# Optimization experiments

Measured on AMD Instinct MI355X. Metric: run time of the kernel, lower is better.

Reference implementation:

```python
import jax, jax.numpy as jnp
import numpy as np


def _normal_distance(n1, n2):
    # Cosine-style normal distance: 1 - <n1, n2>. The original module stubs
    # this as 0; we use the canonical mesh-normal loss so the cdist+argmin+
    # gather chain is exercised end-to-end.
    return 1.0 - jnp.sum(n1 * n2, axis=-1)


def setup_inputs() -> dict:
    key = jax.random.key(0)
    k1, k2, k3, k4 = jax.random.split(key, 4)
    N, M = 8192, 32768
    pred_pts = jax.random.normal(k1, (1, N, 3), dtype=jnp.float32)
    pred_nrm = jax.random.normal(k2, (1, N, 3), dtype=jnp.float32)
    gt_pts = jax.random.normal(k3, (1, M, 3), dtype=jnp.float32)
    gt_nrm = jax.random.normal(k4, (1, M, 3), dtype=jnp.float32)
    # unit normals, as on a real mesh
    pred_nrm = pred_nrm / jnp.linalg.norm(pred_nrm, axis=-1, keepdims=True)
    gt_nrm = gt_nrm / jnp.linalg.norm(gt_nrm, axis=-1, keepdims=True)
    return {
        "predicted_points_batch": pred_pts,
        "predicted_normals_batch": pred_nrm,
        "gt_points_batch": gt_pts,
        "gt_normals_batch": gt_nrm,
    }


def reference(predicted_points_batch, predicted_normals_batch,
              gt_points_batch, gt_normals_batch):
    # Original forward returns inside the first loop iteration -> element 0 only.
    p = predicted_points_batch[0]    # [N,3]
    pn = predicted_normals_batch[0]  # [N,3]
    g = gt_points_batch[0]           # [M,3]
    gn = gt_normals_batch[0]         # [M,3]

    # Squared pairwise distances (monotone in true cdist; only argmin is used).
    # d2[i,j] = |p_i|^2 + |g_j|^2 - 2 p_i . g_j   -> one [N,M] intermediate.
    d2 = (jnp.sum(p * p, axis=1)[:, None]
          + jnp.sum(g * g, axis=1)[None, :]
          - 2.0 * (p @ g.T))                      # [N,M]

    gt_idx = jnp.argmin(d2, axis=1)    # nearest gt point per predicted point, [N]
    pr_idx = jnp.argmin(d2, axis=0)    # nearest predicted point per gt point, [M]

    nearest_gt_normals = gn[gt_idx]    # [N,3]
    nearest_pr_normals = pn[pr_idx]    # [M,3]

    dist1 = _normal_distance(pn, nearest_gt_normals)  # [N]
    dist2 = _normal_distance(gn, nearest_pr_normals)  # [M]
    return jnp.mean(dist1) + jnp.mean(dist2)
```

## Files before the change

### kernel.cpp

```cpp
#include <hip/hip_runtime.h>
#include <stdint.h>
#include <float.h>

#define BLK 256
#define IPT 8
#define OWNERS (BLK * IPT)
#define SLICE 128
#define SUB 64
#define FBLK 64

typedef unsigned long long ull;
typedef float v2f __attribute__((ext_vector_type(2)));

__device__ __forceinline__ v2f fma2(v2f a, v2f b, v2f c) {
    return __builtin_elementwise_fma(a, b, c);
}

__device__ __forceinline__ unsigned int ford(float f) {
    int b = __float_as_int(f);
    return (b >= 0) ? ((unsigned)b ^ 0x80000000u) : ~(unsigned)b;
}
__device__ __forceinline__ float ford_inv(unsigned int u) {
    int b = (u & 0x80000000u) ? (int)(u ^ 0x80000000u) : (int)~u;
    return __int_as_float(b);
}

__global__ __launch_bounds__(BLK) void nn_min_dual(
    const float* __restrict__ p, const float* __restrict__ g,
    ull* __restrict__ rowmin, ull* __restrict__ colmin,
    float* __restrict__ out, int rowBlocks, int rowSlices, int colSlices)
{
    __shared__ float sbx[SLICE], sby[SLICE], sbz[SLICE], sbw[SLICE];

    if (blockIdx.x == 0 && threadIdx.x == 0) *out = 0.0f;

    const float* A; const float* B; ull* outmin; int id, nSlices;
    if ((int)blockIdx.x < rowBlocks) {
        id = blockIdx.x;             A = p; B = g; outmin = rowmin; nSlices = rowSlices;
    } else {
        id = blockIdx.x - rowBlocks; A = g; B = p; outmin = colmin; nSlices = colSlices;
    }
    const int chunk = id / nSlices;
    const int slice = id - chunk * nSlices;
    const int s0 = slice * SLICE;

    if (threadIdx.x < SLICE) {
        int s = s0 + threadIdx.x;
        float bx = B[3 * s], by = B[3 * s + 1], bz = B[3 * s + 2];
        float w = fmaf(bz, bz, fmaf(by, by, bx * bx));
        sbx[threadIdx.x] = bx; sby[threadIdx.x] = by;
        sbz[threadIdx.x] = bz; sbw[threadIdx.x] = w;
    }

    const int o0 = chunk * OWNERS + threadIdx.x;
    v2f ax2[IPT], ay2[IPT], az2[IPT];
    float best[IPT];
    int base[IPT];
#pragma unroll
    for (int r = 0; r < IPT; ++r) {
        int o = o0 + r * BLK;
        float axv = -2.0f * A[3 * o];
        float ayv = -2.0f * A[3 * o + 1];
        float azv = -2.0f * A[3 * o + 2];
        ax2[r] = (v2f){axv, axv};
        ay2[r] = (v2f){ayv, ayv};
        az2[r] = (v2f){azv, azv};
        best[r] = FLT_MAX;
        base[r] = s0;
    }
    __syncthreads();

    for (int st = 0; st < SLICE; st += SUB) {
        float prev[IPT];
#pragma unroll
        for (int r = 0; r < IPT; ++r) prev[r] = best[r];
#pragma unroll 2
        for (int k = st; k < st + SUB; k += 2) {
            v2f qx = *(const v2f*)&sbx[k];
            v2f qy = *(const v2f*)&sby[k];
            v2f qz = *(const v2f*)&sbz[k];
            v2f qw = *(const v2f*)&sbw[k];
#pragma unroll
            for (int r = 0; r < IPT; ++r) {
                v2f t = fma2(az2[r], qz, qw);
                t = fma2(ay2[r], qy, t);
                t = fma2(ax2[r], qx, t);
                best[r] = fminf(fminf(t.x, t.y), best[r]);
            }
        }
#pragma unroll
        for (int r = 0; r < IPT; ++r)
            if (best[r] < prev[r]) base[r] = s0 + st;
    }

#pragma unroll
    for (int r = 0; r < IPT; ++r) {
        ull packed = ((ull)ford(best[r]) << 32) | (unsigned)base[r];
        atomicMin(&outmin[o0 + r * BLK], packed);
    }
}

__global__ __launch_bounds__(FBLK) void finalize_kernel(
    const ull* __restrict__ rowmin, const ull* __restrict__ colmin,
    const float* __restrict__ p, const float* __restrict__ g,
    const float* __restrict__ pn, const float* __restrict__ gn,
    float* __restrict__ out, int N, int M, float invN, float invM)
{
    int t = blockIdx.x * FBLK + threadIdx.x;
    float c = 0.0f;
    if (t < N + M) {
        const float* A; const float* B; const float* An; const float* Bn;
        ull packed; int o; float inv;
        if (t < N) { o = t;     A = p; B = g; An = pn; Bn = gn; packed = rowmin[o]; inv = invN; }
        else       { o = t - N; A = g; B = p; An = gn; Bn = pn; packed = colmin[o]; inv = invM; }

        float ax = -2.0f * A[3 * o];
        float ay = -2.0f * A[3 * o + 1];
        float az = -2.0f * A[3 * o + 2];
        float bestf = ford_inv((unsigned int)(packed >> 32));
        int b0 = (int)(packed & 0xffffffffull);

        int idx = 0x7fffffff;
#pragma unroll 4
        for (int jj = 0; jj < SUB; ++jj) {
            int s = b0 + jj;
            float bx = B[3 * s], by = B[3 * s + 1], bz = B[3 * s + 2];
            float w = fmaf(bz, bz, fmaf(by, by, bx * bx));
            float v = fmaf(ax, bx, fmaf(ay, by, fmaf(az, bz, w)));
            int cand = (v == bestf) ? s : 0x7fffffff;
            idx = (cand < idx) ? cand : idx;
        }
        if (idx == 0x7fffffff) idx = b0;

        float d = An[3 * o] * Bn[3 * idx] + An[3 * o + 1] * Bn[3 * idx + 1]
                + An[3 * o + 2] * Bn[3 * idx + 2];
        c = (1.0f - d) * inv;
    }
#pragma unroll
    for (int off = 32; off > 0; off >>= 1) c += __shfl_down(c, off, 64);
    if (threadIdx.x == 0) atomicAdd(out, c);
}

extern "C" void kernel_launch(void* const* d_in, const int* in_sizes, int n_in,
                              void* d_out, int out_size, void* d_ws, size_t ws_size,
                              hipStream_t stream) {
    const float* p  = (const float*)d_in[0];
    const float* pn = (const float*)d_in[1];
    const float* g  = (const float*)d_in[2];
    const float* gn = (const float*)d_in[3];
    const int N = in_sizes[0] / 3;
    const int M = in_sizes[2] / 3;
    float* out = (float*)d_out;

    ull* rowmin = (ull*)d_ws;
    ull* colmin = rowmin + N;

    hipMemsetAsync(d_ws, 0xFF, (size_t)(N + M) * sizeof(ull), stream);

    const int rowSlices = M / SLICE;
    const int colSlices = N / SLICE;
    const int rowBlocks = (N / OWNERS) * rowSlices;
    const int colBlocks = (M / OWNERS) * colSlices;
    nn_min_dual<<<rowBlocks + colBlocks, BLK, 0, stream>>>(
        p, g, rowmin, colmin, out, rowBlocks, rowSlices, colSlices);

    const int tot = N + M;
    finalize_kernel<<<(tot + FBLK - 1) / FBLK, FBLK, 0, stream>>>(
        rowmin, colmin, p, g, pn, gn, out, N, M, 1.0f / N, 1.0f / M);
}
```

Baseline: 116.0 us.

## Replace atomicMin reduction with per-group partial minima and a reduce pass

The scan kernel now has each block loop over multiple staged slices of the other point set and write its per-owner packed minimum to a dedicated workspace slot instead of issuing global atomicMin. A separate reduce kernel takes the minimum across the K partial groups before the existing exact-index recovery and normal-distance sum. This removes the memset and millions of 64-bit atomics and reduces redundant per-block loading of owner coordinates. In exchange it needs a large workspace and extra reduce-pass reads, and it keeps the old path as a fallback when geometry or workspace size does not fit.

```diff
diff --git a/kernel.cpp b/kernel.cpp
--- a/kernel.cpp
+++ b/kernel.cpp
@@ -5,8 +5,10 @@
 #define BLK 256
 #define IPT 8
 #define OWNERS (BLK * IPT)
-#define SLICE 128
+#define SLICE 256
 #define SUB 64
+#define KROW 64
+#define KCOL 32
 #define FBLK 64
 
 typedef unsigned long long ull;
@@ -25,32 +27,28 @@
     return __int_as_float(b);
 }
 
-__global__ __launch_bounds__(BLK) void nn_min_dual(
-    const float* __restrict__ p, const float* __restrict__ g,
-    ull* __restrict__ rowmin, ull* __restrict__ colmin,
-    float* __restrict__ out, int rowBlocks, int rowSlices, int colSlices)
+__global__ __launch_bounds__(BLK) void nn_scan(
+    const float* __restrict__ p, const float* __restrict__ g,
+    ull* __restrict__ wsR, ull* __restrict__ wsC,
+    float* __restrict__ out, int N, int M)
 {
     __shared__ float sbx[SLICE], sby[SLICE], sbz[SLICE], sbw[SLICE];
 
     if (blockIdx.x == 0 && threadIdx.x == 0) *out = 0.0f;
 
-    const float* A; const float* B; ull* outmin; int id, nSlices;
+    const int rowChunks = N / OWNERS;
+    const int rowBlocks = rowChunks * KROW;
+
+    const float* A; const float* B; ull* ws; int id, nK, NO, cpb;
     if ((int)blockIdx.x < rowBlocks) {
-        id = blockIdx.x;             A = p; B = g; outmin = rowmin; nSlices = rowSlices;
+        id = blockIdx.x;             A = p; B = g; ws = wsR; nK = KROW; NO = N; cpb = M / KROW;
     } else {
-        id = blockIdx.x - rowBlocks; A = g; B = p; outmin = colmin; nSlices = colSlices;
-    }
-    const int chunk = id / nSlices;
-    const int slice = id - chunk * nSlices;
-    const int s0 = slice * SLICE;
-
-    if (threadIdx.x < SLICE) {
-        int s = s0 + threadIdx.x;
-        float bx = B[3 * s], by = B[3 * s + 1], bz = B[3 * s + 2];
-        float w = fmaf(bz, bz, fmaf(by, by, bx * bx));
-        sbx[threadIdx.x] = bx; sby[threadIdx.x] = by;
-        sbz[threadIdx.x] = bz; sbw[threadIdx.x] = w;
-    }
+        id = blockIdx.x - rowBlocks; A = g; B = p; ws = wsC; nK = KCOL; NO = M; cpb = N / KCOL;
+    }
+    const int chunk = id / nK;
+    const int kgrp  = id - chunk * nK;
+    const int c0 = kgrp * cpb;
+    const int nStages = cpb / SLICE;
 
     const int o0 = chunk * OWNERS + threadIdx.x;
     v2f ax2[IPT], ay2[IPT], az2[IPT];
@@ -66,42 +64,54 @@
         ay2[r] = (v2f){ayv, ayv};
         az2[r] = (v2f){azv, azv};
         best[r] = FLT_MAX;
-        base[r] = s0;
-    }
-    __syncthreads();
-
-    for (int st = 0; st < SLICE; st += SUB) {
-        float prev[IPT];
-#pragma unroll
-        for (int r = 0; r < IPT; ++r) prev[r] = best[r];
+        base[r] = c0;
+    }
+
+    for (int stage = 0; stage < nStages; ++stage) {
+        const int gs0 = c0 + stage * SLICE;
+        if (stage) __syncthreads();
+
+        {
+            int s = gs0 + threadIdx.x;
+            float bx = B[3 * s], by = B[3 * s + 1], bz = B[3 * s + 2];
+            float w = fmaf(bz, bz, fmaf(by, by, bx * bx));
+            sbx[threadIdx.x] = bx; sby[threadIdx.x] = by;
+            sbz[threadIdx.x] = bz; sbw[threadIdx.x] = w;
+        }
+        __syncthreads();
+
+        for (int st = 0; st < SLICE; st += SUB) {
+            float prev[IPT];
+#pragma unroll
+            for (int r = 0; r < IPT; ++r) prev[r] = best[r];
 #pragma unroll 2
-        for (int k = st; k < st + SUB; k += 2) {
-            v2f qx = *(const v2f*)&sbx[k];
-            v2f qy = *(const v2f*)&sby[k];
-            v2f qz = *(const v2f*)&sbz[k];
-            v2f qw = *(const v2f*)&sbw[k];
-#pragma unroll
-            for (int r = 0; r < IPT; ++r) {
-                v2f t = fma2(az2[r], qz, qw);
-                t = fma2(ay2[r], qy, t);
-                t = fma2(ax2[r], qx, t);
-                best[r] = fminf(fminf(t.x, t.y), best[r]);
+            for (int k = st; k < st + SUB; k += 2) {
+                v2f qx = *(const v2f*)&sbx[k];
+                v2f qy = *(const v2f*)&sby[k];
+                v2f qz = *(const v2f*)&sbz[k];
+                v2f qw = *(const v2f*)&sbw[k];
+#pragma unroll
+                for (int r = 0; r < IPT; ++r) {
+                    v2f t = fma2(az2[r], qz, qw);
+                    t = fma2(ay2[r], qy, t);
+                    t = fma2(ax2[r], qx, t);
+                    best[r] = fminf(fminf(t.x, t.y), best[r]);
+                }
             }
-        }
-#pragma unroll
-        for (int r = 0; r < IPT; ++r)
-            if (best[r] < prev[r]) base[r] = s0 + st;
-    }
-
-#pragma unroll
-    for (int r = 0; r < IPT; ++r) {
-        ull packed = ((ull)ford(best[r]) << 32) | (unsigned)base[r];
-        atomicMin(&outmin[o0 + r * BLK], packed);
-    }
-}
-
-__global__ __launch_bounds__(FBLK) void finalize_kernel(
-    const ull* __restrict__ rowmin, const ull* __restrict__ colmin,
+#pragma unroll
+            for (int r = 0; r < IPT; ++r)
+                if (best[r] < prev[r]) base[r] = gs0 + st;
+        }
+    }
+
+    ull* dst = ws + (size_t)kgrp * NO;
+#pragma unroll
+    for (int r = 0; r < IPT; ++r)
+        dst[o0 + r * BLK] = ((ull)ford(best[r]) << 32) | (unsigned)base[r];
+}
+
+__global__ __launch_bounds__(FBLK) void nn_reduce(
+    const ull* __restrict__ wsR, const ull* __restrict__ wsC,
     const float* __restrict__ p, const float* __restrict__ g,
     const float* __restrict__ pn, const float* __restrict__ gn,
     float* __restrict__ out, int N, int M, float invN, float invM)
@@ -110,15 +120,22 @@
     float c = 0.0f;
     if (t < N + M) {
         const float* A; const float* B; const float* An; const float* Bn;
-        ull packed; int o; float inv;
-        if (t < N) { o = t;     A = p; B = g; An = pn; Bn = gn; packed = rowmin[o]; inv = invN; }
-        else       { o = t - N; A = g; B = p; An = gn; Bn = pn; packed = colmin[o]; inv = invM; }
+        const ull* ws; int o, K, NO; float inv;
+        if (t < N) { o = t;     A = p; B = g; An = pn; Bn = gn; ws = wsR; K = KROW; NO = N; inv = invN; }
+        else       { o = t - N; A = g; B = p; An = gn; Bn = pn; ws = wsC; K = KCOL; NO = M; inv = invM; }
+
+        ull bestp = ws[o];
+#pragma unroll 4
+        for (int k = 1; k < K; ++k) {
+            ull v2 = ws[(size_t)k * NO + o];
+            bestp = (v2 < bestp) ? v2 : bestp;
+        }
 
         float ax = -2.0f * A[3 * o];
         float ay = -2.0f * A[3 * o + 1];
         float az = -2.0f * A[3 * o + 2];
-        float bestf = ford_inv((unsigned int)(packed >> 32));
-        int b0 = (int)(packed & 0xffffffffull);
+        float bestf = ford_inv((unsigned int)(bestp >> 32));
+        int b0 = (int)(bestp & 0xffffffffull);
 
         int idx = 0x7fffffff;
 #pragma unroll 4
@@ -132,6 +149,105 @@
         }
         if (idx == 0x7fffffff) idx = b0;
 
+        float d = An[3 * o] * Bn[3 * idx] + An[3 * o + 1] * Bn[3 * idx + 1]
+                + An[3 * o + 2] * Bn[3 * idx + 2];
+        c = (1.0f - d) * inv;
+    }
+#pragma unroll
+    for (int off = 32; off > 0; off >>= 1) c += __shfl_down(c, off, 64);
+    if (threadIdx.x == 0) atomicAdd(out, c);
+}
+
+#define L_SLICE 128
+
+__global__ __launch_bounds__(BLK) void nn_min_dual(
+    const float* __restrict__ p, const float* __restrict__ g,
+    ull* __restrict__ rowmin, ull* __restrict__ colmin,
+    float* __restrict__ out, int rowBlocks, int rowSlices, int colSlices)
+{
+    __shared__ float sbx[L_SLICE], sby[L_SLICE], sbz[L_SLICE], sbw[L_SLICE];
+    if (blockIdx.x == 0 && threadIdx.x == 0) *out = 0.0f;
+    const float* A; const float* B; ull* outmin; int id, nSlices;
+    if ((int)blockIdx.x < rowBlocks) {
+        id = blockIdx.x;             A = p; B = g; outmin = rowmin; nSlices = rowSlices;
+    } else {
+        id = blockIdx.x - rowBlocks; A = g; B = p; outmin = colmin; nSlices = colSlices;
+    }
+    const int chunk = id / nSlices;
+    const int slice = id - chunk * nSlices;
+    const int s0 = slice * L_SLICE;
+    if (threadIdx.x < L_SLICE) {
+        int s = s0 + threadIdx.x;
+        float bx = B[3 * s], by = B[3 * s + 1], bz = B[3 * s + 2];
+        float w = fmaf(bz, bz, fmaf(by, by, bx * bx));
+        sbx[threadIdx.x] = bx; sby[threadIdx.x] = by;
+        sbz[threadIdx.x] = bz; sbw[threadIdx.x] = w;
+    }
+    const int o0 = chunk * OWNERS + threadIdx.x;
+    v2f ax2[IPT], ay2[IPT], az2[IPT];
+    float best[IPT]; int base[IPT];
+#pragma unroll
+    for (int r = 0; r < IPT; ++r) {
+        int o = o0 + r * BLK;
+        float axv = -2.0f * A[3 * o], ayv = -2.0f * A[3 * o + 1], azv = -2.0f * A[3 * o + 2];
+        ax2[r] = (v2f){axv, axv}; ay2[r] = (v2f){ayv, ayv}; az2[r] = (v2f){azv, azv};
+        best[r] = FLT_MAX; base[r] = s0;
+    }
+    __syncthreads();
+    for (int st = 0; st < L_SLICE; st += SUB) {
+        float prev[IPT];
+#pragma unroll
+        for (int r = 0; r < IPT; ++r) prev[r] = best[r];
+#pragma unroll 2
+        for (int k = st; k < st + SUB; k += 2) {
+            v2f qx = *(const v2f*)&sbx[k]; v2f qy = *(const v2f*)&sby[k];
+            v2f qz = *(const v2f*)&sbz[k]; v2f qw = *(const v2f*)&sbw[k];
+#pragma unroll
+            for (int r = 0; r < IPT; ++r) {
+                v2f t = fma2(az2[r], qz, qw);
+                t = fma2(ay2[r], qy, t);
+                t = fma2(ax2[r], qx, t);
+                best[r] = fminf(fminf(t.x, t.y), best[r]);
+            }
+        }
+#pragma unroll
+        for (int r = 0; r < IPT; ++r)
+            if (best[r] < prev[r]) base[r] = s0 + st;
+    }
+#pragma unroll
+    for (int r = 0; r < IPT; ++r) {
+        ull packed = ((ull)ford(best[r]) << 32) | (unsigned)base[r];
+        atomicMin(&outmin[o0 + r * BLK], packed);
+    }
+}
+
+__global__ __launch_bounds__(FBLK) void finalize_legacy(
+    const ull* __restrict__ rowmin, const ull* __restrict__ colmin,
+    const float* __restrict__ p, const float* __restrict__ g,
+    const float* __restrict__ pn, const float* __restrict__ gn,
+    float* __restrict__ out, int N, int M, float invN, float invM)
+{
+    int t = blockIdx.x * FBLK + threadIdx.x;
+    float c = 0.0f;
+    if (t < N + M) {
+        const float* A; const float* B; const float* An; const float* Bn;
+        ull packed; int o; float inv;
+        if (t < N) { o = t;     A = p; B = g; An = pn; Bn = gn; packed = rowmin[o]; inv = invN; }
+        else       { o = t - N; A = g; B = p; An = gn; Bn = pn; packed = colmin[o]; inv = invM; }
+        float ax = -2.0f * A[3 * o], ay = -2.0f * A[3 * o + 1], az = -2.0f * A[3 * o + 2];
+        float bestf = ford_inv((unsigned int)(packed >> 32));
+        int b0 = (int)(packed & 0xffffffffull);
+        int idx = 0x7fffffff;
+#pragma unroll 4
+        for (int jj = 0; jj < SUB; ++jj) {
+            int s = b0 + jj;
+            float bx = B[3 * s], by = B[3 * s + 1], bz = B[3 * s + 2];
+            float w = fmaf(bz, bz, fmaf(by, by, bx * bx));
+            float v = fmaf(ax, bx, fmaf(ay, by, fmaf(az, bz, w)));
+            int cand = (v == bestf) ? s : 0x7fffffff;
+            idx = (cand < idx) ? cand : idx;
+        }
+        if (idx == 0x7fffffff) idx = b0;
         float d = An[3 * o] * Bn[3 * idx] + An[3 * o + 1] * Bn[3 * idx + 1]
                 + An[3 * o + 2] * Bn[3 * idx + 2];
         c = (1.0f - d) * inv;
@@ -152,19 +268,32 @@
     const int M = in_sizes[2] / 3;
     float* out = (float*)d_out;
 
-    ull* rowmin = (ull*)d_ws;
-    ull* colmin = rowmin + N;
-
-    hipMemsetAsync(d_ws, 0xFF, (size_t)(N + M) * sizeof(ull), stream);
-
-    const int rowSlices = M / SLICE;
-    const int colSlices = N / SLICE;
-    const int rowBlocks = (N / OWNERS) * rowSlices;
-    const int colBlocks = (M / OWNERS) * colSlices;
-    nn_min_dual<<<rowBlocks + colBlocks, BLK, 0, stream>>>(
-        p, g, rowmin, colmin, out, rowBlocks, rowSlices, colSlices);
-
-    const int tot = N + M;
-    finalize_kernel<<<(tot + FBLK - 1) / FBLK, FBLK, 0, stream>>>(
-        rowmin, colmin, p, g, pn, gn, out, N, M, 1.0f / N, 1.0f / M);
-}
+    const size_t wsRn = (size_t)KROW * N;
+    const size_t wsCn = (size_t)KCOL * M;
+    const size_t needBytes = (wsRn + wsCn) * sizeof(ull);
+
+    const bool geomOK = (N % OWNERS) == 0 && (M % OWNERS) == 0 &&
+                        (M % (KROW * SLICE)) == 0 && (N % (KCOL * SLICE)) == 0 &&
+                        ((N + M) % FBLK) == 0 && (N % FBLK) == 0;
+
+    if (geomOK && ws_size >= needBytes) {
+        ull* wsR = (ull*)d_ws;
+        ull* wsC = wsR + wsRn;
+        const int blocks = (N / OWNERS) * KROW + (M / OWNERS) * KCOL;
+        nn_scan<<<blocks, BLK, 0, stream>>>(p, g, wsR, wsC, out, N, M);
+        nn_reduce<<<(N + M) / FBLK, FBLK, 0, stream>>>(
+            wsR, wsC, p, g, pn, gn, out, N, M, 1.0f / N, 1.0f / M);
+    } else {
+        ull* rowmin = (ull*)d_ws;
+        ull* colmin = rowmin + N;
+        hipMemsetAsync(d_ws, 0xFF, (size_t)(N + M) * sizeof(ull), stream);
+        const int rowSlices = M / L_SLICE;
+        const int colSlices = N / L_SLICE;
+        const int rowBlocks = (N / OWNERS) * rowSlices;
+        const int colBlocks = (M / OWNERS) * colSlices;
+        nn_min_dual<<<rowBlocks + colBlocks, BLK, 0, stream>>>(
+            p, g, rowmin, colmin, out, rowBlocks, rowSlices, colSlices);
+        finalize_legacy<<<(N + M + FBLK - 1) / FBLK, FBLK, 0, stream>>>(
+            rowmin, colmin, p, g, pn, gn, out, N, M, 1.0f / N, 1.0f / M);
+    }
+}
```

Result: slower. 120.7 us (+4.1%).
